# Kernel tuning notes

Hardware: AMD Instinct MI355X
Metric: run time of the kernel (lower is better)

## Reference

```python
import jax, jax.numpy as jnp
import numpy as np

# Multi-scale deformable attention (MSDeformableAttention from RTDETRTransformerv2)
SPATIAL = ((80, 80), (40, 40), (20, 20))  # (h, w) per level, strides 8/16/32 on 640x640
N_HEADS, N_LEVELS, N_POINTS = 8, 3, 4
D_MODEL = 256
HEAD_DIM = D_MODEL // N_HEADS


def setup_inputs() -> dict:
    key = jax.random.key(0)
    ks = jax.random.split(key, 10)
    B, Q = 16, 300
    Lv = sum(h * w for h, w in SPATIAL)  # 8400
    s = 0.02
    return {
        "query": jax.random.normal(ks[0], (B, Q, D_MODEL), jnp.float32),
        "reference_points": jax.random.uniform(ks[1], (B, Q, 4), jnp.float32),
        "value": jax.random.normal(ks[2], (B, Lv, D_MODEL), jnp.float32),
        "Wv": jax.random.normal(ks[3], (D_MODEL, D_MODEL), jnp.float32) * s,
        "bv": jnp.zeros((D_MODEL,), jnp.float32),
        "Woff": jax.random.normal(ks[4], (D_MODEL, N_HEADS * N_LEVELS * N_POINTS * 2), jnp.float32) * s,
        "boff": jax.random.normal(ks[5], (N_HEADS * N_LEVELS * N_POINTS * 2,), jnp.float32) * 0.1,
        "Wattn": jax.random.normal(ks[6], (D_MODEL, N_HEADS * N_LEVELS * N_POINTS), jnp.float32) * s,
        "battn": jnp.zeros((N_HEADS * N_LEVELS * N_POINTS,), jnp.float32),
        "Wout": jax.random.normal(ks[7], (D_MODEL, D_MODEL), jnp.float32) * s,
        "bout": jnp.zeros((D_MODEL,), jnp.float32),
    }


def _grid_sample_level(v_lvl, gx, gy, h, w):
    """Bilinear grid_sample, align_corners=False, zeros padding.

    v_lvl : (B, nH, h*w, hd) flattened per-level value map
    gx,gy : (B, nH, P) sample coords in [-1, 1]
    returns (B, nH, P, hd)
    """
    px = ((gx + 1.0) * w - 1.0) * 0.5  # pixel x
    py = ((gy + 1.0) * h - 1.0) * 0.5  # pixel y
    x0 = jnp.floor(px)
    y0 = jnp.floor(py)
    fx = px - x0
    fy = py - y0
    x0i = x0.astype(jnp.int32)
    y0i = y0.astype(jnp.int32)

    def corner(xi, yi, wgt):
        valid = (xi >= 0) & (xi < w) & (yi >= 0) & (yi < h)
        idx = jnp.clip(yi, 0, h - 1) * w + jnp.clip(xi, 0, w - 1)
        g = jnp.take_along_axis(v_lvl, idx[..., None], axis=2)  # (B,nH,P,hd)
        return g * (wgt * valid.astype(wgt.dtype))[..., None]

    return (corner(x0i, y0i, (1 - fx) * (1 - fy))
            + corner(x0i + 1, y0i, fx * (1 - fy))
            + corner(x0i, y0i + 1, (1 - fx) * fy)
            + corner(x0i + 1, y0i + 1, fx * fy))


def reference(query, reference_points, value, Wv, bv, Woff, boff, Wattn, battn, Wout, bout):
    B, Q, _ = query.shape
    # value projection -> per-head values
    v = (value @ Wv + bv).reshape(B, -1, N_HEADS, HEAD_DIM)
    # sampling offsets and attention weights from queries
    off = (query @ Woff + boff).reshape(B, Q, N_HEADS, N_LEVELS, N_POINTS, 2)
    aw = jax.nn.softmax(
        (query @ Wattn + battn).reshape(B, Q, N_HEADS, N_LEVELS * N_POINTS), axis=-1
    ).reshape(B, Q, N_HEADS, N_LEVELS, N_POINTS)
    # reference points (cx, cy) broadcast over heads/levels/points
    ref = reference_points[:, :, None, None, None, :2]
    pts = jnp.clip(ref + off, 0.0, 1.0)      # (B,Q,nH,nL,nP,2) in [0,1]
    g = pts * 2.0 - 1.0                      # grid_sample coords in [-1,1]

    out = jnp.zeros((B, Q, N_HEADS, HEAD_DIM), query.dtype)
    start = 0
    for lvl, (h, w) in enumerate(SPATIAL):
        v_lvl = v[:, start:start + h * w].transpose(0, 2, 1, 3)  # (B,nH,hw,hd)
        gl = g[:, :, :, lvl]                                     # (B,Q,nH,nP,2)
        gx = gl[..., 0].transpose(0, 2, 1, 3).reshape(B, N_HEADS, Q * N_POINTS)
        gy = gl[..., 1].transpose(0, 2, 1, 3).reshape(B, N_HEADS, Q * N_POINTS)
        sampled = _grid_sample_level(v_lvl, gx, gy, h, w)        # (B,nH,Q*nP,hd)
        sampled = sampled.reshape(B, N_HEADS, Q, N_POINTS, HEAD_DIM)
        wl = aw[:, :, :, lvl].transpose(0, 2, 1, 3)              # (B,nH,Q,nP)
        out = out + jnp.einsum('bhqpd,bhqp->bqhd', sampled, wl)
        start += h * w

    return out.reshape(B, Q, D_MODEL) @ Wout + bout
```

## Files before the change

kernel.cpp:

```cpp
#include <hip/hip_runtime.h>
#include <cstddef>

#define NB 16
#define NQ 300
#define DM 256
#define LV_ 8400

typedef __attribute__((ext_vector_type(8))) short short8;
typedef __attribute__((ext_vector_type(4))) float f32x4;

static __device__ __forceinline__ unsigned short bf16_rne(float f) {
  unsigned int u = __builtin_bit_cast(unsigned int, f);
  u += 0x7FFFu + ((u >> 16) & 1u);
  return (unsigned short)(u >> 16);
}

static __device__ __forceinline__ void split_bf16(float f, short& hi, short& lo) {
  unsigned int u = __builtin_bit_cast(unsigned int, f);
  unsigned int hr = (u + 0x7FFFu + ((u >> 16) & 1u)) & 0xFFFF0000u;
  hi = (short)(hr >> 16);
  float r = f - __builtin_bit_cast(float, hr);
  unsigned int v = __builtin_bit_cast(unsigned int, r);
  lo = (short)((v + 0x7FFFu + ((v >> 16) & 1u)) >> 16);
}

__global__ void wconv_kernel(const float* __restrict__ W,
                             short* __restrict__ Wth, short* __restrict__ Wtl) {
  const int n = blockIdx.x, k = threadIdx.x;
  short h, l;
  split_bf16(W[k * DM + n], h, l);
  Wth[n * DM + k] = h;
  Wtl[n * DM + k] = l;
}

__global__ __launch_bounds__(256) void vproj_mfma(
    const float* __restrict__ A, const short* __restrict__ Wth,
    const short* __restrict__ Wtl, const float* __restrict__ bias,
    unsigned short* __restrict__ V) {
  __shared__ short Ah[4][128][8], Al[4][128][8];
  __shared__ short Bh[4][128][8], Bl[4][128][8];
  const int tid = threadIdx.x;
  const int lane = tid & 63;
  const int wave = tid >> 6;
  const int l16 = lane & 15, q4 = lane >> 4;
  const int wr = (wave >> 1) * 64, wc = (wave & 1) * 64;
  const size_t row0 = (size_t)blockIdx.x * 128;
  const int col0 = blockIdx.y * 128;

  const int arow = tid >> 1;
  const int ahalf = tid & 1;
  const int c0 = ahalf * 2;

  f32x4 acc[4][4];
  #pragma unroll
  for (int i = 0; i < 4; ++i)
    #pragma unroll
    for (int j = 0; j < 4; ++j) acc[i][j] = (f32x4)0.f;

  for (int kk = 0; kk < DM; kk += 32) {
    const float* ap = A + (row0 + arow) * DM + kk + ahalf * 16;
    float4 f0 = *(const float4*)(ap + 0);
    float4 f1 = *(const float4*)(ap + 4);
    float4 f2 = *(const float4*)(ap + 8);
    float4 f3 = *(const float4*)(ap + 12);
    const short* wph = Wth + (size_t)(col0 + arow) * DM + kk + ahalf * 16;
    const short* wpl = Wtl + (size_t)(col0 + arow) * DM + kk + ahalf * 16;
    short8 wh0 = *(const short8*)(wph);
    short8 wh1 = *(const short8*)(wph + 8);
    short8 wl0 = *(const short8*)(wpl);
    short8 wl1 = *(const short8*)(wpl + 8);

    short8 h0, h1, l0, l1;
    const float* ff = (const float*)&f0;
    {
      float tmp[16];
      *(float4*)&tmp[0] = f0; *(float4*)&tmp[4] = f1;
      *(float4*)&tmp[8] = f2; *(float4*)&tmp[12] = f3;
      #pragma unroll
      for (int e = 0; e < 8; ++e) { short h, l; split_bf16(tmp[e], h, l); h0[e] = h; l0[e] = l; }
      #pragma unroll
      for (int e = 0; e < 8; ++e) { short h, l; split_bf16(tmp[8 + e], h, l); h1[e] = h; l1[e] = l; }
    }
    (void)ff;
    __syncthreads();
    *(short8*)&Ah[c0][arow][0] = h0;
    *(short8*)&Ah[c0 + 1][arow][0] = h1;
    *(short8*)&Al[c0][arow][0] = l0;
    *(short8*)&Al[c0 + 1][arow][0] = l1;
    *(short8*)&Bh[c0][arow][0] = wh0;
    *(short8*)&Bh[c0 + 1][arow][0] = wh1;
    *(short8*)&Bl[c0][arow][0] = wl0;
    *(short8*)&Bl[c0 + 1][arow][0] = wl1;
    __syncthreads();

    short8 af[4][2], bf_[4][2];
    #pragma unroll
    for (int i = 0; i < 4; ++i) {
      af[i][0] = *(const short8*)&Ah[q4][wr + i * 16 + l16][0];
      af[i][1] = *(const short8*)&Al[q4][wr + i * 16 + l16][0];
    }
    #pragma unroll
    for (int j = 0; j < 4; ++j) {
      bf_[j][0] = *(const short8*)&Bh[q4][wc + j * 16 + l16][0];
      bf_[j][1] = *(const short8*)&Bl[q4][wc + j * 16 + l16][0];
    }
    #pragma unroll
    for (int i = 0; i < 4; ++i)
      #pragma unroll
      for (int j = 0; j < 4; ++j) {
        acc[i][j] = __builtin_amdgcn_mfma_f32_16x16x32_bf16(af[i][0], bf_[j][0], acc[i][j], 0, 0, 0);
        acc[i][j] = __builtin_amdgcn_mfma_f32_16x16x32_bf16(af[i][1], bf_[j][0], acc[i][j], 0, 0, 0);
        acc[i][j] = __builtin_amdgcn_mfma_f32_16x16x32_bf16(af[i][0], bf_[j][1], acc[i][j], 0, 0, 0);
      }
  }

  #pragma unroll
  for (int i = 0; i < 4; ++i)
    #pragma unroll
    for (int j = 0; j < 4; ++j) {
      const int col = col0 + wc + j * 16 + l16;
      const float bcol = bias[col];
      #pragma unroll
      for (int r = 0; r < 4; ++r) {
        const size_t row = row0 + wr + i * 16 + q4 * 4 + r;
        V[row * DM + col] = bf16_rne(acc[i][j][r] + bcol);
      }
    }
}

__global__ __launch_bounds__(256) void gemm32(
    const float* __restrict__ A, const float* __restrict__ W,
    const float* __restrict__ bias, float* __restrict__ C,
    int M, int N, int K) {
  __shared__ float As[32][34];
  __shared__ float Bs[32][36];
  const int tid = threadIdx.x;
  const int tx = tid & 15, ty = tid >> 4;
  const int m0 = blockIdx.x * 32, n0 = blockIdx.y * 32;
  const int ar = tid & 31, ak = (tid >> 5) * 4;
  const int bk = tid >> 3, bc = (tid & 7) * 4;
  float acc[2][2] = {{0.f, 0.f}, {0.f, 0.f}};
  for (int kk = 0; kk < K; kk += 32) {
    float4 av = *(const float4*)(A + (size_t)(m0 + ar) * K + kk + ak);
    float4 wv = *(const float4*)(W + (size_t)(kk + bk) * N + n0 + bc);
    __syncthreads();
    As[ak + 0][ar] = av.x; As[ak + 1][ar] = av.y;
    As[ak + 2][ar] = av.z; As[ak + 3][ar] = av.w;
    *(float4*)&Bs[bk][bc] = wv;
    __syncthreads();
    #pragma unroll
    for (int k = 0; k < 32; ++k) {
      const float a0 = As[k][ty * 2], a1 = As[k][ty * 2 + 1];
      const float b0 = Bs[k][tx * 2], b1 = Bs[k][tx * 2 + 1];
      acc[0][0] = fmaf(a0, b0, acc[0][0]);
      acc[0][1] = fmaf(a0, b1, acc[0][1]);
      acc[1][0] = fmaf(a1, b0, acc[1][0]);
      acc[1][1] = fmaf(a1, b1, acc[1][1]);
    }
  }
  const float bi0 = bias[n0 + tx * 2], bi1 = bias[n0 + tx * 2 + 1];
  #pragma unroll
  for (int i = 0; i < 2; ++i) {
    float* cp = C + (size_t)(m0 + ty * 2 + i) * N + n0 + tx * 2;
    cp[0] = acc[i][0] + bi0;
    cp[1] = acc[i][1] + bi1;
  }
}

__global__ __launch_bounds__(256) void sample_kernel(
    const float* __restrict__ refp, const unsigned short* __restrict__ v,
    const float* __restrict__ off, const float* __restrict__ logits,
    float* __restrict__ mid) {
  const int bq = blockIdx.x;
  const int b = bq / NQ;
  const int t = threadIdx.x;
  __shared__ float off_sh[192];
  __shared__ float aw_sh[96];
  __shared__ float ref_sh[2];

  if (t < 192) off_sh[t] = off[(size_t)bq * 192 + t];
  else aw_sh[t - 192] = logits[(size_t)bq * 96 + (t - 192)];
  if (t < 32) aw_sh[64 + t] = logits[(size_t)bq * 96 + 64 + t];
  if (t < 2) ref_sh[t] = refp[bq * 4 + t];
  __syncthreads();

  if (t < 8) {
    float m = -1e30f;
    #pragma unroll
    for (int i = 0; i < 12; ++i) m = fmaxf(m, aw_sh[t * 12 + i]);
    float e[12], s = 0.f;
    #pragma unroll
    for (int i = 0; i < 12; ++i) { e[i] = __expf(aw_sh[t * 12 + i] - m); s += e[i]; }
    const float inv = 1.f / s;
    #pragma unroll
    for (int i = 0; i < 12; ++i) aw_sh[t * 12 + i] = e[i] * inv;
  }
  __syncthreads();

  const int h = t >> 5, d = t & 31;
  const float refx = ref_sh[0], refy = ref_sh[1];
  const unsigned short* vb = v + (size_t)b * LV_ * DM + h * 32 + d;
  float acc = 0.f;
  const int LH[3] = {80, 40, 20};
  const int LS[3] = {0, 6400, 8000};
  #pragma unroll
  for (int l = 0; l < 3; ++l) {
    const int hh = LH[l], ww = LH[l], st = LS[l];
    #pragma unroll
    for (int p = 0; p < 4; ++p) {
      const int oi = ((h * 3 + l) * 4 + p) * 2;
      const float aw = aw_sh[h * 12 + l * 4 + p];
      const float sx = fminf(fmaxf(refx + off_sh[oi], 0.f), 1.f);
      const float sy = fminf(fmaxf(refy + off_sh[oi + 1], 0.f), 1.f);
      const float px = sx * (float)ww - 0.5f;
      const float py = sy * (float)hh - 0.5f;
      const float x0f = floorf(px), y0f = floorf(py);
      const float fx = px - x0f, fy = py - y0f;
      const int x0 = (int)x0f, y0 = (int)y0f;
      const int x1 = x0 + 1, y1 = y0 + 1;
      const bool vx0 = (x0 >= 0) & (x0 < ww), vx1 = (x1 >= 0) & (x1 < ww);
      const bool vy0 = (y0 >= 0) & (y0 < hh), vy1 = (y1 >= 0) & (y1 < hh);
      const float w00 = (1.f - fx) * (1.f - fy) * ((vx0 & vy0) ? 1.f : 0.f);
      const float w10 = fx * (1.f - fy) * ((vx1 & vy0) ? 1.f : 0.f);
      const float w01 = (1.f - fx) * fy * ((vx0 & vy1) ? 1.f : 0.f);
      const float w11 = fx * fy * ((vx1 & vy1) ? 1.f : 0.f);
      const int x0c = min(max(x0, 0), ww - 1), x1c = min(max(x1, 0), ww - 1);
      const int y0c = min(max(y0, 0), hh - 1), y1c = min(max(y1, 0), hh - 1);
      const float v00 = __builtin_bit_cast(float, (unsigned int)vb[(size_t)(st + y0c * ww + x0c) * DM] << 16);
      const float v10 = __builtin_bit_cast(float, (unsigned int)vb[(size_t)(st + y0c * ww + x1c) * DM] << 16);
      const float v01 = __builtin_bit_cast(float, (unsigned int)vb[(size_t)(st + y1c * ww + x0c) * DM] << 16);
      const float v11 = __builtin_bit_cast(float, (unsigned int)vb[(size_t)(st + y1c * ww + x1c) * DM] << 16);
      acc += aw * (w00 * v00 + w10 * v10 + w01 * v01 + w11 * v11);
    }
  }
  mid[(size_t)bq * DM + t] = acc;
}

extern "C" void kernel_launch(void* const* d_in, const int* in_sizes, int n_in,
                              void* d_out, int out_size, void* d_ws, size_t ws_size,
                              hipStream_t stream) {
  (void)in_sizes; (void)n_in; (void)out_size; (void)ws_size;
  const float* query = (const float*)d_in[0];
  const float* refp  = (const float*)d_in[1];
  const float* value = (const float*)d_in[2];
  const float* Wv    = (const float*)d_in[3];
  const float* bv    = (const float*)d_in[4];
  const float* Woff  = (const float*)d_in[5];
  const float* boff  = (const float*)d_in[6];
  const float* Wattn = (const float*)d_in[7];
  const float* battn = (const float*)d_in[8];
  const float* Wout  = (const float*)d_in[9];
  const float* bout  = (const float*)d_in[10];
  float* out = (float*)d_out;

  char* ws = (char*)d_ws;
  unsigned short* v_bf = (unsigned short*)ws;
  short* Wth    = (short*)(ws + 68812800);
  short* Wtl    = (short*)(ws + 68943872);
  float* offb   = (float*)(ws + 69074944);
  float* logitb = (float*)(ws + 72761344);
  float* midb   = (float*)(ws + 74604544);

  wconv_kernel<<<DM, DM, 0, stream>>>(Wv, Wth, Wtl);
  vproj_mfma<<<dim3((NB * LV_) / 128, 2), 256, 0, stream>>>(value, Wth, Wtl, bv, v_bf);
  gemm32<<<dim3(4800 / 32, 192 / 32), 256, 0, stream>>>(query, Woff, boff, offb, 4800, 192, 256);
  gemm32<<<dim3(4800 / 32, 96 / 32), 256, 0, stream>>>(query, Wattn, battn, logitb, 4800, 96, 256);
  sample_kernel<<<NB * NQ, 256, 0, stream>>>(refp, v_bf, offb, logitb, midb);
  gemm32<<<dim3(4800 / 32, 256 / 32), 256, 0, stream>>>(midb, Wout, bout, out, 4800, 256, 256);
}
```

Baseline: 352.5 us.

## Use single bf16 MFMA for value projection, larger GEMM tiles, restructure sampling

```diff
diff --git a/kernel.cpp b/kernel.cpp
--- a/kernel.cpp
+++ b/kernel.cpp
@@ -1,4 +1,5 @@
 #include <hip/hip_runtime.h>
+#include <hip/hip_bf16.h>
 #include <cstddef>
 
 #define NB 16
@@ -15,30 +16,24 @@
   return (unsigned short)(u >> 16);
 }
 
-static __device__ __forceinline__ void split_bf16(float f, short& hi, short& lo) {
-  unsigned int u = __builtin_bit_cast(unsigned int, f);
-  unsigned int hr = (u + 0x7FFFu + ((u >> 16) & 1u)) & 0xFFFF0000u;
-  hi = (short)(hr >> 16);
-  float r = f - __builtin_bit_cast(float, hr);
-  unsigned int v = __builtin_bit_cast(unsigned int, r);
-  lo = (short)((v + 0x7FFFu + ((v >> 16) & 1u)) >> 16);
+static __device__ __forceinline__ unsigned int pack_bf2(float a, float b) {
+  __hip_bfloat162 p = __float22bfloat162_rn(make_float2(a, b));
+  unsigned int u;
+  __builtin_memcpy(&u, &p, 4);
+  return u;
 }
 
 __global__ void wconv_kernel(const float* __restrict__ W,
-                             short* __restrict__ Wth, short* __restrict__ Wtl) {
+                             unsigned short* __restrict__ Wth) {
   const int n = blockIdx.x, k = threadIdx.x;
-  short h, l;
-  split_bf16(W[k * DM + n], h, l);
-  Wth[n * DM + k] = h;
-  Wtl[n * DM + k] = l;
+  Wth[n * DM + k] = bf16_rne(W[k * DM + n]);
 }
 
 __global__ __launch_bounds__(256) void vproj_mfma(
-    const float* __restrict__ A, const short* __restrict__ Wth,
-    const short* __restrict__ Wtl, const float* __restrict__ bias,
-    unsigned short* __restrict__ V) {
-  __shared__ short Ah[4][128][8], Al[4][128][8];
-  __shared__ short Bh[4][128][8], Bl[4][128][8];
+    const float* __restrict__ A, const unsigned short* __restrict__ Wth,
+    const float* __restrict__ bias, unsigned short* __restrict__ V) {
+  __shared__ short Ah[4][128][8];
+  __shared__ short Bh[4][128][8];
   const int tid = threadIdx.x;
   const int lane = tid & 63;
   const int wave = tid >> 6;
@@ -48,8 +43,8 @@
   const int col0 = blockIdx.y * 128;
 
   const int arow = tid >> 1;
-  const int ahalf = tid & 1;
-  const int c0 = ahalf * 2;
+  const int half = tid & 1;
+  const int c0 = half * 2;
 
   f32x4 acc[4][4];
   #pragma unroll
@@ -57,61 +52,40 @@
     #pragma unroll
     for (int j = 0; j < 4; ++j) acc[i][j] = (f32x4)0.f;
 
+  const float* ap0 = A + (row0 + arow) * DM + half * 16;
+  const unsigned short* wp0 = Wth + (size_t)(col0 + arow) * DM + half * 16;
+
   for (int kk = 0; kk < DM; kk += 32) {
-    const float* ap = A + (row0 + arow) * DM + kk + ahalf * 16;
-    float4 f0 = *(const float4*)(ap + 0);
-    float4 f1 = *(const float4*)(ap + 4);
-    float4 f2 = *(const float4*)(ap + 8);
-    float4 f3 = *(const float4*)(ap + 12);
-    const short* wph = Wth + (size_t)(col0 + arow) * DM + kk + ahalf * 16;
-    const short* wpl = Wtl + (size_t)(col0 + arow) * DM + kk + ahalf * 16;
-    short8 wh0 = *(const short8*)(wph);
-    short8 wh1 = *(const short8*)(wph + 8);
-    short8 wl0 = *(const short8*)(wpl);
-    short8 wl1 = *(const short8*)(wpl + 8);
-
-    short8 h0, h1, l0, l1;
-    const float* ff = (const float*)&f0;
-    {
-      float tmp[16];
-      *(float4*)&tmp[0] = f0; *(float4*)&tmp[4] = f1;
-      *(float4*)&tmp[8] = f2; *(float4*)&tmp[12] = f3;
-      #pragma unroll
-      for (int e = 0; e < 8; ++e) { short h, l; split_bf16(tmp[e], h, l); h0[e] = h; l0[e] = l; }
-      #pragma unroll
-      for (int e = 0; e < 8; ++e) { short h, l; split_bf16(tmp[8 + e], h, l); h1[e] = h; l1[e] = l; }
-    }
-    (void)ff;
-    __syncthreads();
-    *(short8*)&Ah[c0][arow][0] = h0;
-    *(short8*)&Ah[c0 + 1][arow][0] = h1;
-    *(short8*)&Al[c0][arow][0] = l0;
-    *(short8*)&Al[c0 + 1][arow][0] = l1;
-    *(short8*)&Bh[c0][arow][0] = wh0;
-    *(short8*)&Bh[c0 + 1][arow][0] = wh1;
-    *(short8*)&Bl[c0][arow][0] = wl0;
-    *(short8*)&Bl[c0 + 1][arow][0] = wl1;
-    __syncthreads();
-
-    short8 af[4][2], bf_[4][2];
-    #pragma unroll
-    for (int i = 0; i < 4; ++i) {
-      af[i][0] = *(const short8*)&Ah[q4][wr + i * 16 + l16][0];
-      af[i][1] = *(const short8*)&Al[q4][wr + i * 16 + l16][0];
-    }
-    #pragma unroll
-    for (int j = 0; j < 4; ++j) {
-      bf_[j][0] = *(const short8*)&Bh[q4][wc + j * 16 + l16][0];
-      bf_[j][1] = *(const short8*)&Bl[q4][wc + j * 16 + l16][0];
-    }
+    const float4 f0 = *(const float4*)(ap0 + kk + 0);
+    const float4 f1 = *(const float4*)(ap0 + kk + 4);
+    const float4 f2 = *(const float4*)(ap0 + kk + 8);
+    const float4 f3 = *(const float4*)(ap0 + kk + 12);
+    const uint4 w0 = *(const uint4*)(wp0 + kk);
+    const uint4 w1 = *(const uint4*)(wp0 + kk + 8);
+    uint4 p0, p1;
+    p0.x = pack_bf2(f0.x, f0.y); p0.y = pack_bf2(f0.z, f0.w);
+    p0.z = pack_bf2(f1.x, f1.y); p0.w = pack_bf2(f1.z, f1.w);
+    p1.x = pack_bf2(f2.x, f2.y); p1.y = pack_bf2(f2.z, f2.w);
+    p1.z = pack_bf2(f3.x, f3.y); p1.w = pack_bf2(f3.z, f3.w);
+    __syncthreads();
+    *(uint4*)&Ah[c0][arow][0]     = p0;
+    *(uint4*)&Ah[c0 + 1][arow][0] = p1;
+    *(uint4*)&Bh[c0][arow][0]     = w0;
+    *(uint4*)&Bh[c0 + 1][arow][0] = w1;
+    __syncthreads();
+
+    short8 af[4], bfr[4];
+    #pragma unroll
+    for (int i = 0; i < 4; ++i)
+      af[i] = *(const short8*)&Ah[q4][wr + i * 16 + l16][0];
+    #pragma unroll
+    for (int j = 0; j < 4; ++j)
+      bfr[j] = *(const short8*)&Bh[q4][wc + j * 16 + l16][0];
     #pragma unroll
     for (int i = 0; i < 4; ++i)
       #pragma unroll
-      for (int j = 0; j < 4; ++j) {
-        acc[i][j] = __builtin_amdgcn_mfma_f32_16x16x32_bf16(af[i][0], bf_[j][0], acc[i][j], 0, 0, 0);
-        acc[i][j] = __builtin_amdgcn_mfma_f32_16x16x32_bf16(af[i][1], bf_[j][0], acc[i][j], 0, 0, 0);
-        acc[i][j] = __builtin_amdgcn_mfma_f32_16x16x32_bf16(af[i][0], bf_[j][1], acc[i][j], 0, 0, 0);
-      }
+      for (int j = 0; j < 4; ++j)
+        acc[i][j] = __builtin_amdgcn_mfma_f32_16x16x32_bf16(af[i], bfr[j], acc[i][j], 0, 0, 0);
   }
 
   #pragma unroll
@@ -128,42 +102,62 @@
     }
 }
 
-__global__ __launch_bounds__(256) void gemm32(
+__global__ __launch_bounds__(256) void gemm64(
     const float* __restrict__ A, const float* __restrict__ W,
     const float* __restrict__ bias, float* __restrict__ C,
     int M, int N, int K) {
-  __shared__ float As[32][34];
-  __shared__ float Bs[32][36];
+  __shared__ float As[16][64];
+  __shared__ float Bs[16][64];
   const int tid = threadIdx.x;
   const int tx = tid & 15, ty = tid >> 4;
-  const int m0 = blockIdx.x * 32, n0 = blockIdx.y * 32;
-  const int ar = tid & 31, ak = (tid >> 5) * 4;
-  const int bk = tid >> 3, bc = (tid & 7) * 4;
-  float acc[2][2] = {{0.f, 0.f}, {0.f, 0.f}};
-  for (int kk = 0; kk < K; kk += 32) {
-    float4 av = *(const float4*)(A + (size_t)(m0 + ar) * K + kk + ak);
-    float4 wv = *(const float4*)(W + (size_t)(kk + bk) * N + n0 + bc);
-    __syncthreads();
-    As[ak + 0][ar] = av.x; As[ak + 1][ar] = av.y;
-    As[ak + 2][ar] = av.z; As[ak + 3][ar] = av.w;
-    *(float4*)&Bs[bk][bc] = wv;
-    __syncthreads();
-    #pragma unroll
-    for (int k = 0; k < 32; ++k) {
-      const float a0 = As[k][ty * 2], a1 = As[k][ty * 2 + 1];
-      const float b0 = Bs[k][tx * 2], b1 = Bs[k][tx * 2 + 1];
-      acc[0][0] = fmaf(a0, b0, acc[0][0]);
-      acc[0][1] = fmaf(a0, b1, acc[0][1]);
-      acc[1][0] = fmaf(a1, b0, acc[1][0]);
-      acc[1][1] = fmaf(a1, b1, acc[1][1]);
-    }
-  }
-  const float bi0 = bias[n0 + tx * 2], bi1 = bias[n0 + tx * 2 + 1];
-  #pragma unroll
-  for (int i = 0; i < 2; ++i) {
-    float* cp = C + (size_t)(m0 + ty * 2 + i) * N + n0 + tx * 2;
-    cp[0] = acc[i][0] + bi0;
-    cp[1] = acc[i][1] + bi1;
+  const int m0 = blockIdx.x * 64, n0 = blockIdx.y * 64;
+  const int ar = tid & 63, ak4 = (tid >> 6) * 4;
+  const int bk = tid >> 4, bc4 = (tid & 15) * 4;
+  const int bcol = n0 + bc4;
+
+  float acc[4][4];
+  #pragma unroll
+  for (int i = 0; i < 4; ++i)
+    #pragma unroll
+    for (int j = 0; j < 4; ++j) acc[i][j] = 0.f;
+
+  for (int kk = 0; kk < K; kk += 16) {
+    const float4 av = *(const float4*)(A + (size_t)(m0 + ar) * K + kk + ak4);
+    float4 wv = make_float4(0.f, 0.f, 0.f, 0.f);
+    if (bcol < N) wv = *(const float4*)(W + (size_t)(kk + bk) * N + bcol);
+    __syncthreads();
+    As[ak4 + 0][ar] = av.x;
+    As[ak4 + 1][ar] = av.y;
+    As[ak4 + 2][ar] = av.z;
+    As[ak4 + 3][ar] = av.w;
+    *(float4*)&Bs[bk][bc4] = wv;
+    __syncthreads();
+    #pragma unroll
+    for (int k = 0; k < 16; ++k) {
+      const float4 a4 = *(const float4*)&As[k][ty * 4];
+      const float4 b4 = *(const float4*)&Bs[k][tx * 4];
+      const float* aa = (const float*)&a4;
+      const float* bb = (const float*)&b4;
+      #pragma unroll
+      for (int i = 0; i < 4; ++i)
+        #pragma unroll
+        for (int j = 0; j < 4; ++j)
+          acc[i][j] = fmaf(aa[i], bb[j], acc[i][j]);
+    }
+  }
+
+  if (n0 + tx * 4 < N) {
+    const float4 bi = *(const float4*)&bias[n0 + tx * 4];
+    const float* bb = (const float*)&bi;
+    #pragma unroll
+    for (int i = 0; i < 4; ++i) {
+      float4 o;
+      o.x = acc[i][0] + bb[0];
+      o.y = acc[i][1] + bb[1];
+      o.z = acc[i][2] + bb[2];
+      o.w = acc[i][3] + bb[3];
+      *(float4*)(C + (size_t)(m0 + ty * 4 + i) * N + n0 + tx * 4) = o;
+    }
   }
 }
 
@@ -171,69 +165,90 @@
     const float* __restrict__ refp, const unsigned short* __restrict__ v,
     const float* __restrict__ off, const float* __restrict__ logits,
     float* __restrict__ mid) {
-  const int bq = blockIdx.x;
-  const int b = bq / NQ;
+  const int bq0 = blockIdx.x * 2;
+  const int b = bq0 / NQ;
   const int t = threadIdx.x;
-  __shared__ float off_sh[192];
-  __shared__ float aw_sh[96];
-  __shared__ float ref_sh[2];
-
-  if (t < 192) off_sh[t] = off[(size_t)bq * 192 + t];
-  else aw_sh[t - 192] = logits[(size_t)bq * 96 + (t - 192)];
-  if (t < 32) aw_sh[64 + t] = logits[(size_t)bq * 96 + 64 + t];
-  if (t < 2) ref_sh[t] = refp[bq * 4 + t];
+  __shared__ float off_sh[2][192];
+  __shared__ float aw_sh[2][96];
+  __shared__ int   idx_sh[2][96][4];
+  __shared__ float wt_sh[2][96][4];
+  __shared__ float ref_sh[2][2];
+
+  {
+    const float* osrc = off + (size_t)bq0 * 192;
+    float* odst = &off_sh[0][0];
+    odst[t] = osrc[t];
+    if (t < 128) odst[256 + t] = osrc[256 + t];
+    const float* lsrc = logits + (size_t)bq0 * 96;
+    if (t < 192) (&aw_sh[0][0])[t] = lsrc[t];
+    if (t < 4) ref_sh[t >> 1][t & 1] = refp[(bq0 + (t >> 1)) * 4 + (t & 1)];
+  }
   __syncthreads();
 
-  if (t < 8) {
+  if (t < 16) {
+    const int q = t >> 3, h = t & 7;
+    float* aw = &aw_sh[q][h * 12];
     float m = -1e30f;
     #pragma unroll
-    for (int i = 0; i < 12; ++i) m = fmaxf(m, aw_sh[t * 12 + i]);
+    for (int i = 0; i < 12; ++i) m = fmaxf(m, aw[i]);
     float e[12], s = 0.f;
     #pragma unroll
-    for (int i = 0; i < 12; ++i) { e[i] = __expf(aw_sh[t * 12 + i] - m); s += e[i]; }
+    for (int i = 0; i < 12; ++i) { e[i] = __expf(aw[i] - m); s += e[i]; }
     const float inv = 1.f / s;
     #pragma unroll
-    for (int i = 0; i < 12; ++i) aw_sh[t * 12 + i] = e[i] * inv;
+    for (int i = 0; i < 12; ++i) aw[i] = e[i] * inv;
   }
   __syncthreads();
 
-  const int h = t >> 5, d = t & 31;
-  const float refx = ref_sh[0], refy = ref_sh[1];
-  const unsigned short* vb = v + (size_t)b * LV_ * DM + h * 32 + d;
-  float acc = 0.f;
-  const int LH[3] = {80, 40, 20};
-  const int LS[3] = {0, 6400, 8000};
-  #pragma unroll
-  for (int l = 0; l < 3; ++l) {
+  if (t < 192) {
+    const int q = t / 96, r = t - q * 96;
+    const int h = r / 12, lp = r - h * 12;
+    const int l = lp >> 2, p = lp & 3;
+    const int LH[3] = {80, 40, 20};
+    const int LS[3] = {0, 6400, 8000};
     const int hh = LH[l], ww = LH[l], st = LS[l];
-    #pragma unroll
-    for (int p = 0; p < 4; ++p) {
-      const int oi = ((h * 3 + l) * 4 + p) * 2;
-      const float aw = aw_sh[h * 12 + l * 4 + p];
-      const float sx = fminf(fmaxf(refx + off_sh[oi], 0.f), 1.f);
-      const float sy = fminf(fmaxf(refy + off_sh[oi + 1], 0.f), 1.f);
-      const float px = sx * (float)ww - 0.5f;
-      const float py = sy * (float)hh - 0.5f;
-      const float x0f = floorf(px), y0f = floorf(py);
-      const float fx = px - x0f, fy = py - y0f;
-      const int x0 = (int)x0f, y0 = (int)y0f;
-      const int x1 = x0 + 1, y1 = y0 + 1;
-      const bool vx0 = (x0 >= 0) & (x0 < ww), vx1 = (x1 >= 0) & (x1 < ww);
-      const bool vy0 = (y0 >= 0) & (y0 < hh), vy1 = (y1 >= 0) & (y1 < hh);
-      const float w00 = (1.f - fx) * (1.f - fy) * ((vx0 & vy0) ? 1.f : 0.f);
-      const float w10 = fx * (1.f - fy) * ((vx1 & vy0) ? 1.f : 0.f);
-      const float w01 = (1.f - fx) * fy * ((vx0 & vy1) ? 1.f : 0.f);
-      const float w11 = fx * fy * ((vx1 & vy1) ? 1.f : 0.f);
-      const int x0c = min(max(x0, 0), ww - 1), x1c = min(max(x1, 0), ww - 1);
-      const int y0c = min(max(y0, 0), hh - 1), y1c = min(max(y1, 0), hh - 1);
-      const float v00 = __builtin_bit_cast(float, (unsigned int)vb[(size_t)(st + y0c * ww + x0c) * DM] << 16);
-      const float v10 = __builtin_bit_cast(float, (unsigned int)vb[(size_t)(st + y0c * ww + x1c) * DM] << 16);
-      const float v01 = __builtin_bit_cast(float, (unsigned int)vb[(size_t)(st + y1c * ww + x0c) * DM] << 16);
-      const float v11 = __builtin_bit_cast(float, (unsigned int)vb[(size_t)(st + y1c * ww + x1c) * DM] << 16);
-      acc += aw * (w00 * v00 + w10 * v10 + w01 * v01 + w11 * v11);
-    }
-  }
-  mid[(size_t)bq * DM + t] = acc;
+    const int oi = ((h * 3 + l) * 4 + p) * 2;
+    const float aw = aw_sh[q][h * 12 + lp];
+    const float sx = fminf(fmaxf(ref_sh[q][0] + off_sh[q][oi], 0.f), 1.f);
+    const float sy = fminf(fmaxf(ref_sh[q][1] + off_sh[q][oi + 1], 0.f), 1.f);
+    const float px = sx * (float)ww - 0.5f;
+    const float py = sy * (float)hh - 0.5f;
+    const float x0f = floorf(px), y0f = floorf(py);
+    const float fx = px - x0f, fy = py - y0f;
+    const int x0 = (int)x0f, y0 = (int)y0f;
+    const int x1 = x0 + 1, y1 = y0 + 1;
+    const bool vx0 = (x0 >= 0) & (x0 < ww), vx1 = (x1 >= 0) & (x1 < ww);
+    const bool vy0 = (y0 >= 0) & (y0 < hh), vy1 = (y1 >= 0) & (y1 < hh);
+    const int x0c = min(max(x0, 0), ww - 1), x1c = min(max(x1, 0), ww - 1);
+    const int y0c = min(max(y0, 0), hh - 1), y1c = min(max(y1, 0), hh - 1);
+    idx_sh[q][r][0] = st + y0c * ww + x0c;
+    idx_sh[q][r][1] = st + y0c * ww + x1c;
+    idx_sh[q][r][2] = st + y1c * ww + x0c;
+    idx_sh[q][r][3] = st + y1c * ww + x1c;
+    wt_sh[q][r][0] = aw * (1.f - fx) * (1.f - fy) * ((vx0 & vy0) ? 1.f : 0.f);
+    wt_sh[q][r][1] = aw * fx * (1.f - fy) * ((vx1 & vy0) ? 1.f : 0.f);
+    wt_sh[q][r][2] = aw * (1.f - fx) * fy * ((vx0 & vy1) ? 1.f : 0.f);
+    wt_sh[q][r][3] = aw * fx * fy * ((vx1 & vy1) ? 1.f : 0.f);
+  }
+  __syncthreads();
+
+  const int q = t >> 7, h = (t >> 4) & 7, dp = t & 15;
+  const unsigned short* vb = v + (size_t)b * LV_ * DM + h * 32 + dp * 2;
+  float ax = 0.f, ay = 0.f;
+  #pragma unroll
+  for (int r = 0; r < 12; ++r) {
+    const int rr = h * 12 + r;
+    #pragma unroll
+    for (int c = 0; c < 4; ++c) {
+      const int id = idx_sh[q][rr][c];
+      const float w = wt_sh[q][rr][c];
+      const unsigned int u = *(const unsigned int*)(vb + (size_t)id * DM);
+      ax = fmaf(w, __builtin_bit_cast(float, u << 16), ax);
+      ay = fmaf(w, __builtin_bit_cast(float, u & 0xFFFF0000u), ay);
+    }
+  }
+  float2 o; o.x = ax; o.y = ay;
+  *(float2*)(mid + (size_t)(bq0 + q) * DM + h * 32 + dp * 2) = o;
 }
 
 extern "C" void kernel_launch(void* const* d_in, const int* in_sizes, int n_in,
@@ -255,16 +270,15 @@
 
   char* ws = (char*)d_ws;
   unsigned short* v_bf = (unsigned short*)ws;
-  short* Wth    = (short*)(ws + 68812800);
-  short* Wtl    = (short*)(ws + 68943872);
-  float* offb   = (float*)(ws + 69074944);
-  float* logitb = (float*)(ws + 72761344);
-  float* midb   = (float*)(ws + 74604544);
-
-  wconv_kernel<<<DM, DM, 0, stream>>>(Wv, Wth, Wtl);
-  vproj_mfma<<<dim3((NB * LV_) / 128, 2), 256, 0, stream>>>(value, Wth, Wtl, bv, v_bf);
-  gemm32<<<dim3(4800 / 32, 192 / 32), 256, 0, stream>>>(query, Woff, boff, offb, 4800, 192, 256);
-  gemm32<<<dim3(4800 / 32, 96 / 32), 256, 0, stream>>>(query, Wattn, battn, logitb, 4800, 96, 256);
-  sample_kernel<<<NB * NQ, 256, 0, stream>>>(refp, v_bf, offb, logitb, midb);
-  gemm32<<<dim3(4800 / 32, 256 / 32), 256, 0, stream>>>(midb, Wout, bout, out, 4800, 256, 256);
-}
+  unsigned short* Wth  = (unsigned short*)(ws + 68812800);
+  float* offb   = (float*)(ws + 68943872);
+  float* logitb = (float*)(ws + 72630272);
+  float* midb   = (float*)(ws + 74473472);
+
+  wconv_kernel<<<DM, DM, 0, stream>>>(Wv, Wth);
+  vproj_mfma<<<dim3((NB * LV_) / 128, 2), 256, 0, stream>>>(value, Wth, bv, v_bf);
+  gemm64<<<dim3(75, 3), 256, 0, stream>>>(query, Woff, boff, offb, 4800, 192, 256);
+  gemm64<<<dim3(75, 2), 256, 0, stream>>>(query, Wattn, battn, logitb, 4800, 96, 256);
+  sample_kernel<<<2400, 256, 0, stream>>>(refp, v_bf, offb, logitb, midb);
+  gemm64<<<dim3(75, 4), 256, 0, stream>>>(midb, Wout, bout, out, 4800, 256, 256);
+}
```

Result: no change. 347.3 us (-1.5%).
